# Optimization experiments

Hardware: AMD Instinct MI355X
Metric: run time of the kernel (lower is better)

Reference implementation:

```python
import jax, jax.numpy as jnp
import numpy as np

B, C, S, D = 16, 32, 64, 512
DFF, E = 2048, 8


def setup_inputs() -> dict:
    key = jax.random.key(0)
    ks = jax.random.split(key, 16)
    std = 0.02
    return {
        'x': jax.random.normal(ks[0], (B, C, S, D), jnp.float32),
        'baseline': jax.random.normal(ks[1], (B, C, S, D), jnp.float32),
        'attnres': jax.random.normal(ks[2], (B, C, S, D), jnp.float32),
        'shared_w1': jax.random.normal(ks[3], (DFF, D), jnp.float32) * std,
        'shared_b1': jnp.zeros((DFF,), jnp.float32),
        'shared_w2': jax.random.normal(ks[4], (D, DFF), jnp.float32) * std,
        'shared_b2': jnp.zeros((D,), jnp.float32),
        'spa_router_w': jax.random.normal(ks[5], (E, 3 * D), jnp.float32) * std,
        'spa_router_b': jnp.zeros((E,), jnp.float32),
        'spe_router_w': jax.random.normal(ks[6], (E, 3 * D), jnp.float32) * std,
        'spe_router_b': jnp.zeros((E,), jnp.float32),
        'spa_w1': jax.random.normal(ks[7], (E, DFF, D), jnp.float32) * std,
        'spa_b1': jnp.zeros((E, DFF), jnp.float32),
        'spa_w2': jax.random.normal(ks[8], (E, D, DFF), jnp.float32) * std,
        'spa_b2': jnp.zeros((E, D), jnp.float32),
        'spe_w1': jax.random.normal(ks[9], (E, DFF, D), jnp.float32) * std,
        'spe_b1': jnp.zeros((E, DFF), jnp.float32),
        'spe_w2': jax.random.normal(ks[10], (E, D, DFF), jnp.float32) * std,
        'spe_b2': jnp.zeros((E, D), jnp.float32),
    }


def _route(feat, rw, rb):
    # feat [B, 3D] -> top-1 expert index [B] and its softmax gate weight [B]
    logits = feat @ rw.T + rb            # [B, E]
    p = jax.nn.softmax(logits, axis=-1)
    idx = jnp.argmax(logits, axis=-1)    # [B]
    w = jnp.take_along_axis(p, idx[:, None], axis=-1)[:, 0]
    return idx, w


def _specialist(xf, idx, w1, b1, w2, b2):
    # xf [B, T, D]; per-sample gather of expert weights then batched FFN
    W1, B1 = w1[idx], b1[idx]            # [B, DFF, D], [B, DFF]
    W2, B2 = w2[idx], b2[idx]            # [B, D, DFF], [B, D]
    h = jax.nn.gelu(jnp.einsum('btd,bfd->btf', xf, W1) + B1[:, None, :])
    return jnp.einsum('btf,bdf->btd', h, W2) + B2[:, None, :]


def reference(x, baseline, attnres, shared_w1, shared_b1, shared_w2, shared_b2,
              spa_router_w, spa_router_b, spe_router_w, spe_router_b,
              spa_w1, spa_b1, spa_w2, spa_b2, spe_w1, spe_b1, spe_w2, spe_b2):
    b, d = x.shape[0], x.shape[-1]
    xf = x.reshape(b, -1, d)  # [B, T, D]
    # sample-level AttnRes router features: [B, 3*d_model]
    feat = jnp.concatenate([
        baseline.mean(axis=(1, 2)),
        attnres.mean(axis=(1, 2)),
        (attnres - baseline).mean(axis=(1, 2)),
    ], axis=-1)
    spa_idx, spa_w = _route(feat, spa_router_w, spa_router_b)
    spe_idx, spe_w = _route(feat, spe_router_w, spe_router_b)
    # shared dense FFN (dropout=0 eval)
    shared = jax.nn.gelu(xf @ shared_w1.T + shared_b1) @ shared_w2.T + shared_b2
    spa_out = _specialist(xf, spa_idx, spa_w1, spa_b1, spa_w2, spa_b2)
    spe_out = _specialist(xf, spe_idx, spe_w1, spe_b1, spe_w2, spe_b2)
    y = shared + spa_w[:, None, None] * spa_out + spe_w[:, None, None] * spe_out
    return y.reshape(x.shape)
```

## Files before the change

kernel.cpp:

```cpp
#include <hip/hip_runtime.h>
#include <cstdint>
#include <cstddef>

#define DEV __device__ __forceinline__

typedef unsigned short u16;
typedef _Float16 f16x8 __attribute__((ext_vector_type(8)));
typedef float f32x4 __attribute__((ext_vector_type(4)));

static constexpr int NB  = 16;
static constexpr int T   = 2048;
static constexpr int D   = 512;
static constexpr int DFF = 2048;
static constexpr int NE  = 8;
static constexpr int FEAT = 3 * D;

#define MFMA16 __builtin_amdgcn_mfma_f32_16x16x32_f16

DEV u16 f2h(float f) {
  _Float16 h = (_Float16)f;
  union { _Float16 h; u16 u; } cv; cv.h = h; return cv.u;
}

DEV float gelu_fast(float x) {
  const float t = x * x;
  const float p = x * fmaf(t, -0.07135481627f, -1.59576912161f);
  return __fdividef(x, 1.0f + __expf(p));
}


__global__ void k_part(const float* __restrict__ base, const float* __restrict__ attn,
                       float* __restrict__ part) {
  const int b = blockIdx.x >> 4, ch = blockIdx.x & 15;
  const int d = threadIdx.x;
  const size_t o = ((size_t)b * T + (size_t)ch * 128) * D + d;
  const float* pb = base + o;
  const float* pa = attn + o;
  float sb = 0.f, sa = 0.f;
  for (int r = 0; r < 128; ++r) { sb += pb[(size_t)r * D]; sa += pa[(size_t)r * D]; }
  part[(b * 16 + ch) * D + d] = sb;
  part[NB * 16 * D + (b * 16 + ch) * D + d] = sa;
}

__global__ void k_router(const float* __restrict__ part,
                         const float* __restrict__ rw0, const float* __restrict__ rb0,
                         const float* __restrict__ rw1, const float* __restrict__ rb1,
                         const float* __restrict__ b2s, const float* __restrict__ b2a,
                         const float* __restrict__ b2e,
                         int* __restrict__ idx, float* __restrict__ gate,
                         float* __restrict__ btot) {
  __shared__ float fsh[FEAT];
  __shared__ float lgsh[2][8];
  __shared__ int   sidx[2];
  __shared__ float sgate[2];
  const int b = blockIdx.x, t = threadIdx.x;

  float sb = 0.f, sa = 0.f;
  for (int ch = 0; ch < 16; ++ch) {
    sb += part[(b * 16 + ch) * D + t];
    sa += part[NB * 16 * D + (b * 16 + ch) * D + t];
  }
  sb *= (1.0f / 2048.0f); sa *= (1.0f / 2048.0f);
  fsh[t] = sb; fsh[D + t] = sa; fsh[2 * D + t] = sa - sb;
  __syncthreads();

  const int wid = t >> 6, lane = t & 63;
  for (int pair = wid; pair < 16; pair += 8) {
    const int r = pair >> 3, e = pair & 7;
    const float* rw = r ? rw1 : rw0;
    float p = 0.f;
    for (int k = lane; k < FEAT; k += 64) p += fsh[k] * rw[e * FEAT + k];
#pragma unroll
    for (int off = 32; off >= 1; off >>= 1) p += __shfl_xor(p, off);
    if (lane == 0) lgsh[r][e] = p + (r ? rb1[e] : rb0[e]);
  }
  __syncthreads();

  if (t < 2) {
    const int r = t;
    float best = -1e30f; int bi = 0;
#pragma unroll
    for (int e = 0; e < 8; ++e)
      if (lgsh[r][e] > best) { best = lgsh[r][e]; bi = e; }
    float s = 0.f;
#pragma unroll
    for (int e = 0; e < 8; ++e) s += expf(lgsh[r][e] - best);
    sidx[r] = bi; sgate[r] = 1.0f / s;
    idx[r * 16 + b] = bi;
    gate[r * 16 + b] = 1.0f / s;
  }
  __syncthreads();

  const int ia = sidx[0], ie = sidx[1];
  const float ga = sgate[0], ge = sgate[1];
  btot[b * D + t] = b2s[t] + ga * b2a[ia * D + t] + ge * b2e[ie * D + t];
}


DEV void cast4(const float* __restrict__ s, u16* __restrict__ d, long i) {
  const float4 v = *(const float4*)(s + i);
  const unsigned int lo = (unsigned int)f2h(v.x) | ((unsigned int)f2h(v.y) << 16);
  const unsigned int hi = (unsigned int)f2h(v.z) | ((unsigned int)f2h(v.w) << 16);
  *(uint2*)(d + i) = make_uint2(lo, hi);
}

__global__ void k_cast3(const float* __restrict__ x, const float* __restrict__ sw1,
                        const float* __restrict__ sw2, u16* __restrict__ xh,
                        u16* __restrict__ w1s, u16* __restrict__ w2s) {
  const long NX = (long)NB * T * D;
  const long NW = (long)DFF * D;
  const long t = ((long)blockIdx.x * 256 + threadIdx.x) * 4;
  if (t < NX)               cast4(x,   xh,  t);
  else if (t < NX + NW)     cast4(sw1, w1s, t - NX);
  else                      cast4(sw2, w2s, t - NX - NW);
}

__global__ void k_castg(const float* __restrict__ aw1, const float* __restrict__ aw2,
                        const float* __restrict__ ew1, const float* __restrict__ ew2,
                        u16* __restrict__ w1a, u16* __restrict__ w2a,
                        u16* __restrict__ w1e, u16* __restrict__ w2e,
                        const int* __restrict__ idx) {
  const int rg = blockIdx.x >> 13;
  const int e  = (blockIdx.x >> 10) & 7;
  const int ro = (rg >= 2) ? 16 : 0;
  bool used = false;
#pragma unroll
  for (int i = 0; i < 16; ++i) used |= (idx[ro + i] == e);
  if (!used) return;
  const long i = (long)e * (DFF * D) + ((long)(blockIdx.x & 1023) * 256 + threadIdx.x) * 4;
  const float* s = (rg == 0) ? aw1 : (rg == 1) ? aw2 : (rg == 2) ? ew1 : ew2;
  u16*         d = (rg == 0) ? w1a : (rg == 1) ? w2a : (rg == 2) ? w1e : w2e;
  cast4(s, d, i);
}


DEV void ld_lds16(const void* g, void* l) {
  __builtin_amdgcn_global_load_lds((const __attribute__((address_space(1))) void*)g,
                                   (__attribute__((address_space(3))) void*)l, 16, 0, 0);
}

#define BAR __builtin_amdgcn_s_barrier()
#define LGKM0 do { asm volatile("s_waitcnt lgkmcnt(0)" ::: "memory"); \
                   __builtin_amdgcn_sched_barrier(0); } while (0)
#define VMW2 asm volatile("s_waitcnt vmcnt(2)" ::: "memory")
#define VMW0 asm volatile("s_waitcnt vmcnt(0)" ::: "memory")


#define STG_A(tt, h, sb) do { const long ko_ = (long)(tt) * 64;                          \
    ld_lds16(((h) ? gA10 : gA00) + ko_, (char*)As + (sb) * 32768 + (h) * 16384 + dR0);   \
    ld_lds16(((h) ? gA11 : gA01) + ko_, (char*)As + (sb) * 32768 + (h) * 16384 + dR1); } while (0)
#define STG_B(tt, h, sb) do { const long ko_ = (long)(tt) * 64;                          \
    ld_lds16(((h) ? gB10 : gB00) + ko_, (char*)Bs + (sb) * 32768 + (h) * 16384 + dR0);   \
    ld_lds16(((h) ? gB11 : gB01) + ko_, (char*)Bs + (sb) * 32768 + (h) * 16384 + dR1); } while (0)

#define RD_A(dst, mb, sb) do {                                                           \
    _Pragma("unroll") for (int m_ = 0; m_ < 4; ++m_)                                     \
      _Pragma("unroll") for (int k_ = 0; k_ < 2; ++k_)                                   \
        dst[m_][k_] = *(const f16x8*)((const char*)As + (sb) * 32768 + avb[k_] +         \
                                      ((mb) + m_) * 2048); } while (0)
#define RD_B(dst, nb, sb) do {                                                           \
    _Pragma("unroll") for (int n_ = 0; n_ < 2; ++n_)                                     \
      _Pragma("unroll") for (int k_ = 0; k_ < 2; ++k_)                                   \
        dst[n_][k_] = *(const f16x8*)((const char*)Bs + (sb) * 32768 + bvb[k_] +         \
                                      ((nb) + n_) * 2048); } while (0)

#define QUAD(av, bv, mb, nb) do { __builtin_amdgcn_s_setprio(1);                         \
    _Pragma("unroll") for (int m_ = 0; m_ < 4; ++m_)                                     \
      _Pragma("unroll") for (int n_ = 0; n_ < 2; ++n_) {                                 \
        acc[(mb)+m_][(nb)+n_] = MFMA16(av[m_][0], bv[n_][0], acc[(mb)+m_][(nb)+n_],0,0,0); \
        acc[(mb)+m_][(nb)+n_] = MFMA16(av[m_][1], bv[n_][1], acc[(mb)+m_][(nb)+n_],0,0,0); \
      }                                                                                  \
    __builtin_amdgcn_s_setprio(0); } while (0)

#define TILE(tt, sb, STGN, STGA0, VMN) do {                                              \
    RD_A(avLO, 0, sb); RD_B(bvA, 0, sb);                                                 \
    if (STGN) { STG_A((tt)+1, 1, (sb)^1); STG_B((tt)+1, 0, (sb)^1); STG_B((tt)+1, 1, (sb)^1); } \
    BAR; LGKM0; QUAD(avLO, bvA, 0, 0); BAR;                                              \
    RD_B(bvB, 2, sb);                                                                    \
    BAR; LGKM0; QUAD(avLO, bvB, 0, 2); BAR;                                              \
    RD_A(avHI, 4, sb);                                                                   \
    BAR; LGKM0; QUAD(avHI, bvB, 4, 2); BAR;                                              \
    if (STGA0) STG_A((tt)+2, 0, sb);                                                     \
    BAR; __builtin_amdgcn_sched_barrier(0); QUAD(avHI, bvA, 4, 0);                       \
    if ((VMN) == 2) VMW2; else if ((VMN) == 0) VMW0;                                     \
    BAR;                                                                                 \
  } while (0)

template <int NT>
DEV void gemm_8p(const u16* __restrict__ A, int lda, const u16* __restrict__ B, int ldb,
                 u16* As, u16* Bs, f32x4 (&acc)[8][4]) {
  static_assert(NT >= 8 && (NT % 2) == 0, "NT even, >= 8");
  const int tid = threadIdx.x;
  const int lane = tid & 63, wid = tid >> 6;
  const int wr = wid >> 2, wc = wid & 3;

  const int srow = lane >> 3;
  const int scol = (lane & 7) ^ srow;
  const int rj0 = wid * 16 + srow;
  const int rj1 = rj0 + 8;
  const u16* gA00 = A + (size_t)(  0 + rj0) * lda + scol * 8;
  const u16* gA01 = A + (size_t)(  0 + rj1) * lda + scol * 8;
  const u16* gA10 = A + (size_t)(128 + rj0) * lda + scol * 8;
  const u16* gA11 = A + (size_t)(128 + rj1) * lda + scol * 8;
  const u16* gB00 = B + (size_t)(  0 + rj0) * ldb + scol * 8;
  const u16* gB01 = B + (size_t)(  0 + rj1) * ldb + scol * 8;
  const u16* gB10 = B + (size_t)(128 + rj0) * ldb + scol * 8;
  const u16* gB11 = B + (size_t)(128 + rj1) * ldb + scol * 8;
  const int dR0 = (wid * 16) * 128;
  const int dR1 = dR0 + 1024;

  const int aR = wr * 128 + (lane & 15);
  const int bR = wc * 64 + (lane & 15);
  const int sH = lane >> 4;
  int avb[2], bvb[2];
#pragma unroll
  for (int k_ = 0; k_ < 2; ++k_) {
    const int s_ = (k_ * 4 + sH);
    avb[k_] = aR * 128 + ((s_ ^ (lane & 7)) * 16);
    bvb[k_] = bR * 128 + ((s_ ^ (lane & 7)) * 16);
  }

  f16x8 avLO[4][2], avHI[4][2], bvA[2][2], bvB[2][2];

  STG_A(0, 0, 0); STG_A(0, 1, 0); STG_B(0, 0, 0); STG_B(0, 1, 0);
  STG_A(1, 0, 1);
  VMW2; BAR;

  for (int tp = 0; tp < (NT - 2) / 2; ++tp) {
    TILE(2 * tp,     0, true, true, 2);
    TILE(2 * tp + 1, 1, true, true, 2);
  }
  TILE(NT - 2, 0, true,  false, 0);
  TILE(NT - 1, 1, false, false, -1);
}


#define STG2_A(tt, h, sb) do { const long ko_ = (long)(tt) * 64;                         \
    ld_lds16(((h) ? qA10 : qA00) + ko_, (char*)As2 + (sb) * 16384 + (h) * 8192 + dQ0);   \
    ld_lds16(((h) ? qA11 : qA01) + ko_, (char*)As2 + (sb) * 16384 + (h) * 8192 + dQ1); } while (0)
#define STG2_B(tt, h, sb) do { const long ko_ = (long)(tt) * 64;                         \
    ld_lds16(((h) ? qB10 : qB00) + ko_, (char*)Bs2 + (sb) * 16384 + (h) * 8192 + dQ0);   \
    ld_lds16(((h) ? qB11 : qB01) + ko_, (char*)Bs2 + (sb) * 16384 + (h) * 8192 + dQ1); } while (0)

#define RD2_A(dst, mb, sb) do {                                                          \
    _Pragma("unroll") for (int m_ = 0; m_ < 2; ++m_)                                     \
      _Pragma("unroll") for (int k_ = 0; k_ < 2; ++k_)                                   \
        dst[m_][k_] = *(const f16x8*)((const char*)As2 + (sb) * 16384 + avb[k_] +        \
                                      ((mb) + m_) * 2048); } while (0)
#define RD2_B(dst, nb, sb) do {                                                          \
    _Pragma("unroll") for (int n_ = 0; n_ < 2; ++n_)                                     \
      _Pragma("unroll") for (int k_ = 0; k_ < 2; ++k_)                                   \
        dst[n_][k_] = *(const f16x8*)((const char*)Bs2 + (sb) * 16384 + bvb[k_] +        \
                                      ((nb) + n_) * 2048); } while (0)

#define QUAD2(av, bv, mb, nb) do { __builtin_amdgcn_s_setprio(1);                        \
    _Pragma("unroll") for (int m_ = 0; m_ < 2; ++m_)                                     \
      _Pragma("unroll") for (int n_ = 0; n_ < 2; ++n_) {                                 \
        acc[(mb)+m_][(nb)+n_] = MFMA16(av[m_][0], bv[n_][0], acc[(mb)+m_][(nb)+n_],0,0,0); \
        acc[(mb)+m_][(nb)+n_] = MFMA16(av[m_][1], bv[n_][1], acc[(mb)+m_][(nb)+n_],0,0,0); \
      }                                                                                  \
    __builtin_amdgcn_s_setprio(0); } while (0)

#define TILE2(tt, sb, STGN, STGA0, VMN) do {                                             \
    RD2_A(avLO, 0, sb); RD2_B(bvA, 0, sb);                                               \
    if (STGN) { STG2_A((tt)+1, 1, (sb)^1); STG2_B((tt)+1, 0, (sb)^1); STG2_B((tt)+1, 1, (sb)^1); } \
    BAR; LGKM0; QUAD2(avLO, bvA, 0, 0); BAR;                                             \
    RD2_B(bvB, 2, sb);                                                                   \
    BAR; LGKM0; QUAD2(avLO, bvB, 0, 2); BAR;                                             \
    RD2_A(avHI, 2, sb);                                                                  \
    BAR; LGKM0; QUAD2(avHI, bvB, 2, 2); BAR;                                             \
    if (STGA0) STG2_A((tt)+2, 0, sb);                                                    \
    BAR; __builtin_amdgcn_sched_barrier(0); QUAD2(avHI, bvA, 2, 0);                      \
    if ((VMN) == 2) VMW2; else if ((VMN) == 0) VMW0;                                     \
    BAR;                                                                                 \
  } while (0)

template <int BANK>
__global__ __launch_bounds__(256) void k_ffn1(
    const u16* __restrict__ xh, const u16* __restrict__ w1, const float* __restrict__ b1,
    const int* __restrict__ idx, const float* __restrict__ gate, u16* __restrict__ h) {
  __shared__ alignas(16) u16 As2[2 * 8192];
  __shared__ alignas(16) u16 Bs2[2 * 8192];
  int wg = blockIdx.x;
  const int q = (int)gridDim.x >> 3;
  wg = (wg & 7) * q + (wg >> 3);
  const int b  = wg >> 8;
  const int mt = (wg >> 4) & 15;
  const int nt = wg & 15;

  const int e   = (BANK == 0) ? 0 : idx[(BANK - 1) * 16 + b];
  const float g = (BANK == 0) ? 1.0f : gate[(BANK - 1) * 16 + b];
  const u16* A = xh + ((size_t)b * T + (size_t)mt * 128) * D;
  const u16* B = w1 + (size_t)e * DFF * D + (size_t)nt * 128 * D;
  const float* bb = b1 + (size_t)e * DFF;

  const int tid = threadIdx.x;
  const int lane = tid & 63, wid = tid >> 6;
  const int wr = wid >> 1, wc = wid & 1;

  const int srow = lane >> 3;
  const int scol = (lane & 7) ^ srow;
  const int r0 = wid * 8 + srow;
  const u16* qA00 = A + (size_t)(  0 + r0) * D + scol * 8;
  const u16* qA01 = A + (size_t)( 32 + r0) * D + scol * 8;
  const u16* qA10 = A + (size_t)( 64 + r0) * D + scol * 8;
  const u16* qA11 = A + (size_t)( 96 + r0) * D + scol * 8;
  const u16* qB00 = B + (size_t)(  0 + r0) * D + scol * 8;
  const u16* qB01 = B + (size_t)( 32 + r0) * D + scol * 8;
  const u16* qB10 = B + (size_t)( 64 + r0) * D + scol * 8;
  const u16* qB11 = B + (size_t)( 96 + r0) * D + scol * 8;
  const int dQ0 = wid * 1024;
  const int dQ1 = dQ0 + 4096;

  const int aR = wr * 64 + (lane & 15);
  const int bR = wc * 64 + (lane & 15);
  const int sH = lane >> 4;
  int avb[2], bvb[2];
#pragma unroll
  for (int k_ = 0; k_ < 2; ++k_) {
    const int s_ = (k_ * 4 + sH);
    avb[k_] = aR * 128 + ((s_ ^ (aR & 7)) * 16);
    bvb[k_] = bR * 128 + ((s_ ^ (bR & 7)) * 16);
  }

  f32x4 acc[4][4];
#pragma unroll
  for (int m = 0; m < 4; ++m)
#pragma unroll
    for (int n = 0; n < 4; ++n)
#pragma unroll
      for (int r = 0; r < 4; ++r) acc[m][n][r] = 0.f;

  f16x8 avLO[2][2], avHI[2][2], bvA[2][2], bvB[2][2];

  STG2_A(0, 0, 0); STG2_A(0, 1, 0); STG2_B(0, 0, 0); STG2_B(0, 1, 0);
  STG2_A(1, 0, 1);
  VMW2; BAR;

  TILE2(0, 0, true, true, 2);
  TILE2(1, 1, true, true, 2);
  TILE2(2, 0, true, true, 2);
  TILE2(3, 1, true, true, 2);
  TILE2(4, 0, true, true, 2);
  TILE2(5, 1, true, true, 2);
  TILE2(6, 0, true,  false, 0);
  TILE2(7, 1, false, false, -1);

  const int rr = (lane >> 4) << 2, cc = lane & 15;
  const int mrow = mt * 128 + wr * 64;
  const int ncol = nt * 128 + wc * 64;
  u16* hb = h + (size_t)b * T * DFF;
  u16* wsl = (u16*)As2 + wid * 1152;
  const int rdrow = lane >> 2;
  const int rdcb  = lane & 3;
  float bias[4];
#pragma unroll
  for (int n = 0; n < 4; ++n) bias[n] = bb[ncol + n * 16 + cc];
#pragma unroll
  for (int m = 0; m < 4; ++m) {
#pragma unroll
    for (int n = 0; n < 4; ++n) {
      const f32x4 a = acc[m][n];
#pragma unroll
      for (int r = 0; r < 4; ++r)
        wsl[(rr + r) * 72 + n * 16 + cc] = f2h(gelu_fast(a[r] + bias[n]) * g);
    }
    asm volatile("s_waitcnt lgkmcnt(0)" ::: "memory");
    __builtin_amdgcn_sched_barrier(0);
    const uint4 v0 = *(const uint4*)(wsl + rdrow * 72 + rdcb * 16);
    const uint4 v1 = *(const uint4*)(wsl + rdrow * 72 + rdcb * 16 + 8);
    u16* dst = hb + (size_t)(mrow + m * 16 + rdrow) * DFF + ncol + rdcb * 16;
    *(uint4*)dst = v0;
    *(uint4*)(dst + 8) = v1;
    asm volatile("s_waitcnt lgkmcnt(0)" ::: "memory");
    __builtin_amdgcn_sched_barrier(0);
  }
}

template <int BANK>
__global__ __launch_bounds__(512) void k_ffn2(
    const u16* __restrict__ h, const u16* __restrict__ w2, const float* __restrict__ btot,
    const int* __restrict__ idx, float* __restrict__ out) {
  __shared__ alignas(16) u16 As[2 * 16384];
  __shared__ alignas(16) u16 Bs[2 * 16384];
  int wg = blockIdx.x;
  const int q = (int)gridDim.x >> 3;
  wg = (wg & 7) * q + (wg >> 3);
  const int b  = wg >> 4;
  const int mt = (wg >> 1) & 7;
  const int nt = wg & 1;

  const int e = (BANK == 0) ? 0 : idx[(BANK - 1) * 16 + b];
  const u16* Ab = h + ((size_t)b * T + (size_t)mt * 256) * DFF;
  const u16* Bb = w2 + (size_t)e * D * DFF + (size_t)nt * 256 * DFF;

  f32x4 acc[8][4];
#pragma unroll
  for (int m = 0; m < 8; ++m)
#pragma unroll
    for (int n = 0; n < 4; ++n)
#pragma unroll
      for (int r = 0; r < 4; ++r) acc[m][n][r] = 0.f;

  gemm_8p<32>(Ab, DFF, Bb, DFF, As, Bs, acc);

  const int lane = threadIdx.x & 63, wid = threadIdx.x >> 6;
  const int wr = wid >> 2, wc = wid & 3;
  const int rr = (lane >> 4) << 2, cc = lane & 15;
  const int mrow = mt * 256 + wr * 128;
  const int ncol = nt * 256 + wc * 64;
  float* ob = out + (size_t)b * T * D;
  float* wsl = (float*)(void*)As + wid * (16 * 68);
  float btv[4];
#pragma unroll
  for (int n = 0; n < 4; ++n)
    btv[n] = (BANK == 0) ? btot[b * D + ncol + n * 16 + cc] : 0.f;
#pragma unroll
  for (int m = 0; m < 8; ++m) {
#pragma unroll
    for (int n = 0; n < 4; ++n) {
      const f32x4 a = acc[m][n];
#pragma unroll
      for (int r = 0; r < 4; ++r)
        wsl[(rr + r) * 68 + n * 16 + cc] = a[r] + btv[n];
    }
    asm volatile("s_waitcnt lgkmcnt(0)" ::: "memory");
    __builtin_amdgcn_sched_barrier(0);
#pragma unroll
    for (int j = 0; j < 4; ++j) {
      const int row = j * 4 + (lane >> 4);
      const int colb = lane & 15;
      f32x4 v = *(const f32x4*)(wsl + row * 68 + colb * 4);
      float* dst = ob + (size_t)(mrow + m * 16 + row) * D + ncol + colb * 4;
      if (BANK != 0) { const f32x4 o = *(const f32x4*)dst; v += o; }
      *(f32x4*)dst = v;
    }
    asm volatile("s_waitcnt lgkmcnt(0)" ::: "memory");
    __builtin_amdgcn_sched_barrier(0);
  }
}


extern "C" void kernel_launch(void* const* d_in, const int* in_sizes, int n_in,
                              void* d_out, int out_size, void* d_ws, size_t ws_size,
                              hipStream_t stream) {
  (void)in_sizes; (void)n_in; (void)out_size; (void)ws_size;
  const float* x    = (const float*)d_in[0];
  const float* base = (const float*)d_in[1];
  const float* attn = (const float*)d_in[2];
  const float* sw1  = (const float*)d_in[3];
  const float* sb1  = (const float*)d_in[4];
  const float* sw2  = (const float*)d_in[5];
  const float* sb2  = (const float*)d_in[6];
  const float* arw  = (const float*)d_in[7];
  const float* arb  = (const float*)d_in[8];
  const float* erw  = (const float*)d_in[9];
  const float* erb  = (const float*)d_in[10];
  const float* aw1  = (const float*)d_in[11];
  const float* ab1  = (const float*)d_in[12];
  const float* aw2  = (const float*)d_in[13];
  const float* ab2  = (const float*)d_in[14];
  const float* ew1  = (const float*)d_in[15];
  const float* eb1  = (const float*)d_in[16];
  const float* ew2  = (const float*)d_in[17];
  const float* eb2  = (const float*)d_in[18];
  float* out = (float*)d_out;

  char* w = (char*)d_ws;
  u16* xh   = (u16*)w;  w += (size_t)NB * T * D * 2;
  u16* hbuf = (u16*)w;  w += (size_t)NB * T * DFF * 2;
  u16* w1s  = (u16*)w;  w += (size_t)DFF * D * 2;
  u16* w2s  = (u16*)w;  w += (size_t)D * DFF * 2;
  u16* w1a  = (u16*)w;  w += (size_t)NE * DFF * D * 2;
  u16* w2a  = (u16*)w;  w += (size_t)NE * D * DFF * 2;
  u16* w1e  = (u16*)w;  w += (size_t)NE * DFF * D * 2;
  u16* w2e  = (u16*)w;  w += (size_t)NE * D * DFF * 2;
  float* part = (float*)w; w += (size_t)2 * NB * 16 * D * 4;
  int*   idx  = (int*)w;   w += 32 * 4;
  float* gate = (float*)w; w += 32 * 4;
  float* btot = (float*)w; w += (size_t)NB * D * 4;

  k_part<<<dim3(256), dim3(512), 0, stream>>>(base, attn, part);
  k_router<<<dim3(16), dim3(512), 0, stream>>>(part, arw, arb, erw, erb,
                                               sb2, ab2, eb2, idx, gate, btot);

  k_cast3<<<dim3(18432), 256, 0, stream>>>(x, sw1, sw2, xh, w1s, w2s);
  k_castg<<<dim3(32768), 256, 0, stream>>>(aw1, aw2, ew1, ew2, w1a, w2a, w1e, w2e, idx);

  const dim3 g1(4096), g2(256), blk1(256), blk2(512);
  k_ffn1<0><<<g1, blk1, 0, stream>>>(xh, w1s, sb1, idx, gate, hbuf);
  k_ffn2<0><<<g2, blk2, 0, stream>>>(hbuf, w2s, btot, idx, out);
  k_ffn1<1><<<g1, blk1, 0, stream>>>(xh, w1a, ab1, idx, gate, hbuf);
  k_ffn2<1><<<g2, blk2, 0, stream>>>(hbuf, w2a, btot, idx, out);
  k_ffn1<2><<<g1, blk1, 0, stream>>>(xh, w1e, eb1, idx, gate, hbuf);
  k_ffn2<2><<<g2, blk2, 0, stream>>>(hbuf, w2e, btot, idx, out);
}
```

Measured before the change: 708.0 us.

## Prefetch full K-tiles two steps ahead in both GEMM pipelines

Reworks the double-buffered LDS pipeline in both GEMM paths. The full A and B tiles for step t+1 are now staged in the prologue, and each tile issues the loads for step t+2 into the buffer it is consuming, after the relevant LDS reads. The wait threshold moves from vmcnt(2) to vmcnt(8), so more global loads stay in flight and load latency is hidden further ahead. The risk is a write-after-read hazard on the same LDS buffer: correctness depends on the barriers ordering every wave's reads before the overwrite.

```diff
diff --git a/kernel.cpp b/kernel.cpp
--- a/kernel.cpp
+++ b/kernel.cpp
@@ -142,7 +142,7 @@
 #define BAR __builtin_amdgcn_s_barrier()
 #define LGKM0 do { asm volatile("s_waitcnt lgkmcnt(0)" ::: "memory"); \
                    __builtin_amdgcn_sched_barrier(0); } while (0)
-#define VMW2 asm volatile("s_waitcnt vmcnt(2)" ::: "memory")
+#define VMW8 asm volatile("s_waitcnt vmcnt(8)" ::: "memory")
 #define VMW0 asm volatile("s_waitcnt vmcnt(0)" ::: "memory")
 
 
@@ -172,17 +172,17 @@
       }                                                                                  \
     __builtin_amdgcn_s_setprio(0); } while (0)
 
-#define TILE(tt, sb, STGN, STGA0, VMN) do {                                              \
+#define TILE(tt, sb, STGN, VMN) do {                                                     \
     RD_A(avLO, 0, sb); RD_B(bvA, 0, sb);                                                 \
-    if (STGN) { STG_A((tt)+1, 1, (sb)^1); STG_B((tt)+1, 0, (sb)^1); STG_B((tt)+1, 1, (sb)^1); } \
     BAR; LGKM0; QUAD(avLO, bvA, 0, 0); BAR;                                              \
     RD_B(bvB, 2, sb);                                                                    \
     BAR; LGKM0; QUAD(avLO, bvB, 0, 2); BAR;                                              \
     RD_A(avHI, 4, sb);                                                                   \
+    if (STGN) { STG_B((tt)+2, 0, sb); STG_B((tt)+2, 1, sb); }                            \
     BAR; LGKM0; QUAD(avHI, bvB, 4, 2); BAR;                                              \
-    if (STGA0) STG_A((tt)+2, 0, sb);                                                     \
+    if (STGN) { STG_A((tt)+2, 0, sb); STG_A((tt)+2, 1, sb); }                            \
     BAR; __builtin_amdgcn_sched_barrier(0); QUAD(avHI, bvA, 4, 0);                       \
-    if ((VMN) == 2) VMW2; else if ((VMN) == 0) VMW0;                                     \
+    if ((VMN) == 8) VMW8; else if ((VMN) == 0) VMW0;                                     \
     BAR;                                                                                 \
   } while (0)
 
@@ -223,15 +223,15 @@
   f16x8 avLO[4][2], avHI[4][2], bvA[2][2], bvB[2][2];
 
   STG_A(0, 0, 0); STG_A(0, 1, 0); STG_B(0, 0, 0); STG_B(0, 1, 0);
-  STG_A(1, 0, 1);
-  VMW2; BAR;
+  STG_A(1, 0, 1); STG_A(1, 1, 1); STG_B(1, 0, 1); STG_B(1, 1, 1);
+  VMW8; BAR;
 
   for (int tp = 0; tp < (NT - 2) / 2; ++tp) {
-    TILE(2 * tp,     0, true, true, 2);
-    TILE(2 * tp + 1, 1, true, true, 2);
-  }
-  TILE(NT - 2, 0, true,  false, 0);
-  TILE(NT - 1, 1, false, false, -1);
+    TILE(2 * tp,     0, true, 8);
+    TILE(2 * tp + 1, 1, true, 8);
+  }
+  TILE(NT - 2, 0, false, 0);
+  TILE(NT - 1, 1, false, -1);
 }
 
 
@@ -261,17 +261,17 @@
       }                                                                                  \
     __builtin_amdgcn_s_setprio(0); } while (0)
 
-#define TILE2(tt, sb, STGN, STGA0, VMN) do {                                             \
+#define TILE2(tt, sb, STGN, VMN) do {                                                    \
     RD2_A(avLO, 0, sb); RD2_B(bvA, 0, sb);                                               \
-    if (STGN) { STG2_A((tt)+1, 1, (sb)^1); STG2_B((tt)+1, 0, (sb)^1); STG2_B((tt)+1, 1, (sb)^1); } \
     BAR; LGKM0; QUAD2(avLO, bvA, 0, 0); BAR;                                             \
     RD2_B(bvB, 2, sb);                                                                   \
     BAR; LGKM0; QUAD2(avLO, bvB, 0, 2); BAR;                                             \
     RD2_A(avHI, 2, sb);                                                                  \
+    if (STGN) { STG2_B((tt)+2, 0, sb); STG2_B((tt)+2, 1, sb); }                          \
     BAR; LGKM0; QUAD2(avHI, bvB, 2, 2); BAR;                                             \
-    if (STGA0) STG2_A((tt)+2, 0, sb);                                                    \
+    if (STGN) { STG2_A((tt)+2, 0, sb); STG2_A((tt)+2, 1, sb); }                          \
     BAR; __builtin_amdgcn_sched_barrier(0); QUAD2(avHI, bvA, 2, 0);                      \
-    if ((VMN) == 2) VMW2; else if ((VMN) == 0) VMW0;                                     \
+    if ((VMN) == 8) VMW8; else if ((VMN) == 0) VMW0;                                     \
     BAR;                                                                                 \
   } while (0)
 
@@ -334,17 +334,17 @@
   f16x8 avLO[2][2], avHI[2][2], bvA[2][2], bvB[2][2];
 
   STG2_A(0, 0, 0); STG2_A(0, 1, 0); STG2_B(0, 0, 0); STG2_B(0, 1, 0);
-  STG2_A(1, 0, 1);
-  VMW2; BAR;
-
-  TILE2(0, 0, true, true, 2);
-  TILE2(1, 1, true, true, 2);
-  TILE2(2, 0, true, true, 2);
-  TILE2(3, 1, true, true, 2);
-  TILE2(4, 0, true, true, 2);
-  TILE2(5, 1, true, true, 2);
-  TILE2(6, 0, true,  false, 0);
-  TILE2(7, 1, false, false, -1);
+  STG2_A(1, 0, 1); STG2_A(1, 1, 1); STG2_B(1, 0, 1); STG2_B(1, 1, 1);
+  VMW8; BAR;
+
+  TILE2(0, 0, true, 8);
+  TILE2(1, 1, true, 8);
+  TILE2(2, 0, true, 8);
+  TILE2(3, 1, true, 8);
+  TILE2(4, 0, true, 8);
+  TILE2(5, 1, true, 8);
+  TILE2(6, 0, false, 0);
+  TILE2(7, 1, false, -1);
 
   const int rr = (lane >> 4) << 2, cc = lane & 15;
   const int mrow = mt * 128 + wr * 64;
```

Measured after the change: 672.1 us. 5.1% less time.
